# Kernel optimization log

Measured on AMD Instinct MI355X. Metric: run time of the kernel, lower is better.

Reference implementation:

```python
import jax, jax.numpy as jnp
import numpy as np

N_NODES = 100_000
N_FACES = 200_000
N_EDGES1 = 800_000
N_TRIP = 500_000
H = 64
GEO_IN = 10 + 2 * 23  # 56
N_INTER = 3
DEPTH = 3  # finaldepth; total SPNN layers = DEPTH + 1
PI = float(np.pi)
EPS = 1e-5


def setup_inputs() -> dict:
    key = jax.random.key(0)
    ks = jax.random.split(key, 12)
    s = 0.05
    input_feature = jax.random.normal(ks[0], (N_NODES, H), jnp.float32)
    coords = jax.random.normal(ks[1], (N_NODES, 3), jnp.float32)
    face_norm = jax.random.normal(ks[2], (N_FACES, 3), jnp.float32)
    face_x = jax.random.normal(ks[3], (N_FACES, 23), jnp.float32)
    edge_whichface = jax.random.randint(ks[4], (N_EDGES1,), 0, N_FACES)
    edge_index_2rd = jax.random.randint(ks[5], (3, N_TRIP), 0, N_NODES)
    edx_ij = jax.random.randint(ks[6], (N_TRIP,), 0, N_EDGES1)
    edx_rand = jax.random.randint(ks[7], (N_TRIP,), 0, N_EDGES1)
    edx_jk = jnp.where(jnp.arange(N_TRIP) % 2 == 0, edx_ij, edx_rand)
    att = jnp.ones((2,), jnp.float32)
    W_geo = jax.random.normal(ks[8], (H, GEO_IN), jnp.float32) * s
    b_geo = jnp.zeros((H,), jnp.float32)
    g_geo = jnp.ones((H,), jnp.float32)
    be_geo = jnp.zeros((H,), jnp.float32)
    spnn_W0 = jax.random.normal(ks[9], (N_INTER, 2, H, 4 * H), jnp.float32) * s
    spnn_b0 = jnp.zeros((N_INTER, 2, H), jnp.float32)
    spnn_Wr = jax.random.normal(ks[10], (N_INTER, 2, DEPTH, H, H), jnp.float32) * s
    spnn_br = jnp.zeros((N_INTER, 2, DEPTH, H), jnp.float32)
    bn_g = jnp.ones((N_INTER, 2, DEPTH + 1, H), jnp.float32)
    bn_b = jnp.zeros((N_INTER, 2, DEPTH + 1, H), jnp.float32)
    return dict(input_feature=input_feature, coords=coords, face_norm=face_norm,
                face_x=face_x, att=att, W_geo=W_geo, b_geo=b_geo, g_geo=g_geo,
                be_geo=be_geo, spnn_W0=spnn_W0, spnn_b0=spnn_b0, spnn_Wr=spnn_Wr,
                spnn_br=spnn_br, bn_g=bn_g, bn_b=bn_b,
                edge_whichface=edge_whichface, edge_index_2rd=edge_index_2rd,
                edx_jk=edx_jk, edx_ij=edx_ij)


def _bn(x, g, b):
    # BatchNorm1d, training mode (batch stats, biased variance)
    mean = x.mean(0)
    var = ((x - mean) ** 2).mean(0)
    return (x - mean) * jax.lax.rsqrt(var + EPS) * g + b


def _masked_bn(x, mf, g, b):
    # BatchNorm over only the masked rows (original code runs BN on x_i[mask]);
    # applied to all rows, masked rows selected afterward -> identical math.
    cnt = jnp.maximum(mf.sum(), 1.0)
    mean = (x * mf).sum(0) / cnt
    var = (((x - mean) ** 2) * mf).sum(0) / cnt
    return (x - mean) * jax.lax.rsqrt(var + EPS) * g + b


def _angle(v1, v2):
    c = jnp.cross(v1, v2)
    return jnp.arctan2(jnp.linalg.norm(c, axis=1), (v1 * v2).sum(1))


def reference(input_feature, coords, face_norm, face_x, att, W_geo, b_geo,
              g_geo, be_geo, spnn_W0, spnn_b0, spnn_Wr, spnn_br, bn_g, bn_b,
              edge_whichface, edge_index_2rd, edx_jk, edx_ij):
    i, j, k = edge_index_2rd
    f_ij = edge_whichface[edx_ij]
    f_jk = edge_whichface[edx_jk]
    # angle_face is computed then multiplied by 0 in the original
    angle_face = (PI - _angle(face_norm[f_ij], face_norm[f_jk])) * 0.0
    cj, ci, ck = coords[j], coords[i], coords[k]
    d_ij = jnp.linalg.norm(cj - ci, axis=1)
    d_jk = jnp.linalg.norm(cj - ck, axis=1)
    theta = _angle(cj - ci, ck - cj)
    same_face = f_ij == f_jk
    geo = jnp.concatenate([d_ij[:, None], d_jk[:, None], theta[:, None],
                           angle_face[:, None], cj, ci,
                           face_x[f_ij], face_x[f_jk]], axis=-1)  # [E, 56]
    geo = jax.nn.relu(_bn(geo @ W_geo.T + b_geo, g_geo, be_geo))  # [E, H]

    nf = input_feature
    masks = [same_face, ~same_face]
    outs = []
    for t in range(N_INTER):
        xcat = jnp.concatenate([nf[i], nf[j], nf[k], geo], axis=-1)  # [E, 4H]
        x_out = jnp.zeros((xcat.shape[0], H), xcat.dtype)
        for bi in range(2):
            mf = masks[bi].astype(xcat.dtype)[:, None]
            x = jax.nn.relu(_masked_bn(xcat @ spnn_W0[t, bi].T + spnn_b0[t, bi],
                                       mf, bn_g[t, bi, 0], bn_b[t, bi, 0]))
            for l in range(DEPTH):
                x = jax.nn.relu(_masked_bn(x @ spnn_Wr[t, bi, l].T + spnn_br[t, bi, l],
                                           mf, bn_g[t, bi, l + 1], bn_b[t, bi, l + 1]))
            x = jax.nn.leaky_relu(x) * att[bi]
            x_out = x_out + x * mf
        nf = jax.ops.segment_sum(x_out, i, num_segments=N_NODES)
        outs.append(nf)
    return jnp.stack(outs)  # [N_INTER, N, H] (list in original)
```

## Files before the change

kernel.cpp:

```cpp
#include <hip/hip_runtime.h>

#define E_TRIP 500000
#define EPAD   500224
#define NTILE64 (EPAD/64)
#define NBLK256 (EPAD/256)
#define NBLK    1954
#define NN 100000
#define EPSF 1e-5f
#define RSTAT 64

typedef _Float16 f16;
typedef _Float16 f16x8 __attribute__((ext_vector_type(8)));
typedef float f32x4 __attribute__((ext_vector_type(4)));

__global__ __launch_bounds__(256) void k_count(const int* __restrict__ ewf,
    const int* __restrict__ exij, const int* __restrict__ exjk,
    unsigned char* __restrict__ biedge, int* __restrict__ cb0)
{
  __shared__ int wcnt[4];
  int e = blockIdx.x*256 + threadIdx.x;
  bool active = e < E_TRIP;
  int b = 0;
  if (active) {
    int fij = ewf[exij[e]];
    int fjk = ewf[exjk[e]];
    b = (fij == fjk) ? 0 : 1;
    biedge[e] = (unsigned char)b;
  }
  unsigned long long m0 = __ballot(active && b==0);
  int lane = threadIdx.x & 63, wv = threadIdx.x >> 6;
  if (lane == 0) wcnt[wv] = (int)__popcll(m0);
  __syncthreads();
  if (threadIdx.x == 0) cb0[blockIdx.x] = wcnt[0] + wcnt[1] + wcnt[2] + wcnt[3];
}

__global__ __launch_bounds__(1024) void k_scanb(const int* __restrict__ cb0,
    int* __restrict__ base0, int* __restrict__ base1, int* __restrict__ sc)
{
  __shared__ int s[2048];
  int tid = threadIdx.x;
  int i0 = tid, i1 = tid + 1024;
  s[i0] = (i0 < NBLK) ? cb0[i0] : 0;
  s[i1] = (i1 < NBLK) ? cb0[i1] : 0;
  __syncthreads();
  for (int off = 1; off < 2048; off <<= 1) {
    int v0 = (i0 >= off) ? s[i0 - off] : 0;
    int v1 = (i1 >= off) ? s[i1 - off] : 0;
    __syncthreads();
    s[i0] += v0; s[i1] += v1;
    __syncthreads();
  }
  int c0 = s[NBLK-1];
  int c0p = (c0 + 63) & ~63;
  if (tid == 0) { sc[4] = c0; sc[5] = c0p; sc[6] = E_TRIP - c0; }
  for (int i = tid; i < NBLK; i += 1024) {
    int incl = s[i];
    int ex0 = incl - cb0[i];
    int active_before = i*256; if (active_before > E_TRIP) active_before = E_TRIP;
    base0[i] = ex0;
    base1[i] = c0p + (active_before - ex0);
  }
}

__global__ __launch_bounds__(256) void k_partition(const unsigned char* __restrict__ biedge,
    const int* __restrict__ eidx, const int* __restrict__ base0, const int* __restrict__ base1,
    int* __restrict__ epos, int* __restrict__ ip, int* __restrict__ jp, int* __restrict__ kp)
{
  __shared__ int w0[4], w1[4];
  int e = blockIdx.x*256 + threadIdx.x;
  bool active = e < E_TRIP;
  int b = active ? (int)biedge[e] : 0;
  unsigned long long m0 = __ballot(active && b==0);
  unsigned long long m1 = __ballot(active && b==1);
  int lane = threadIdx.x & 63, wv = threadIdx.x >> 6;
  if (lane == 0) { w0[wv] = (int)__popcll(m0); w1[wv] = (int)__popcll(m1); }
  __syncthreads();
  int off0 = 0, off1 = 0;
  #pragma unroll
  for (int w = 0; w < 4; w++) if (w < wv) { off0 += w0[w]; off1 += w1[w]; }
  if (active) {
    unsigned long long m = b ? m1 : m0;
    unsigned pre = __builtin_amdgcn_mbcnt_lo((unsigned)m, 0u);
    pre = __builtin_amdgcn_mbcnt_hi((unsigned)(m >> 32), pre);
    int base = b ? (base1[blockIdx.x] + off1) : (base0[blockIdx.x] + off0);
    int pos = base + (int)pre;
    epos[pos] = e;
    ip[pos] = eidx[e];
    jp[pos] = eidx[E_TRIP + e];
    kp[pos] = eidx[2*E_TRIP + e];
  }
}

__global__ __launch_bounds__(256) void k_cvt(const float* __restrict__ W0,
    const float* __restrict__ Wr, const float* __restrict__ nf,
    f16* __restrict__ W0h, f16* __restrict__ Wrh, f16* __restrict__ nfh)
{
  int i = blockIdx.x*256 + threadIdx.x;
  if (i < 98304) W0h[i] = (f16)W0[i];
  else if (i < 98304 + 73728) Wrh[i - 98304] = (f16)Wr[i - 98304];
  else { int j = i - 172032; if (j < NN*64) nfh[j] = (f16)nf[j]; }
}

__global__ __launch_bounds__(256) void k_hist(const int* __restrict__ ip,
    const int* __restrict__ sc, int* __restrict__ cnt)
{
  int p = blockIdx.x*256 + threadIdx.x;
  int c0 = sc[4], c0p = sc[5], c1 = sc[6];
  bool valid = (p < c0) || (p >= c0p && p < c0p + c1);
  if (valid) atomicAdd(&cnt[ip[p]], 1);
}

__global__ __launch_bounds__(512) void k_scan1(const int* __restrict__ cnt,
    int* __restrict__ start, int* __restrict__ btot)
{
  __shared__ int s[512];
  int tid = threadIdx.x;
  int g = blockIdx.x*512 + tid;
  int x = (g < NN) ? cnt[g] : 0;
  s[tid] = x; __syncthreads();
  #pragma unroll
  for (int off = 1; off < 512; off <<= 1) {
    int v = (tid >= off) ? s[tid-off] : 0;
    __syncthreads();
    s[tid] += v;
    __syncthreads();
  }
  if (g < NN) start[g] = s[tid] - x;
  if (tid == 511) btot[blockIdx.x] = s[511];
}

__global__ __launch_bounds__(256) void k_scan2(int* __restrict__ btot)
{
  __shared__ int s[256];
  int tid = threadIdx.x;
  int x = (tid < 196) ? btot[tid] : 0;
  s[tid] = x; __syncthreads();
  #pragma unroll
  for (int off = 1; off < 256; off <<= 1) {
    int v = (tid >= off) ? s[tid-off] : 0;
    __syncthreads();
    s[tid] += v;
    __syncthreads();
  }
  if (tid < 196) btot[tid] = s[tid] - x;
}

__global__ __launch_bounds__(512) void k_scan3(int* __restrict__ start,
    int* __restrict__ cur, const int* __restrict__ btot, const int* __restrict__ sc)
{
  int tid = threadIdx.x;
  int g = blockIdx.x*512 + tid;
  if (g < NN) {
    int v = start[g] + btot[blockIdx.x];
    start[g] = v;
    cur[g] = v;
  }
  if (g == 0) start[NN] = sc[4] + sc[6];
}

__global__ __launch_bounds__(256) void k_place(const int* __restrict__ ip,
    const int* __restrict__ sc, int* __restrict__ cur, int* __restrict__ dperm)
{
  int p = blockIdx.x*256 + threadIdx.x;
  int c0 = sc[4], c0p = sc[5], c1 = sc[6];
  bool valid = (p < c0) || (p >= c0p && p < c0p + c1);
  if (valid) {
    int pos = atomicAdd(&cur[ip[p]], 1);
    dperm[pos] = p;
  }
}

__global__ __launch_bounds__(256) void k_geo(
    const float* __restrict__ coords, const float* __restrict__ facex,
    const int* __restrict__ ewf, const int* __restrict__ exij, const int* __restrict__ exjk,
    const float* __restrict__ Wgeo, const float* __restrict__ bgeo,
    const int* __restrict__ sc, const int* __restrict__ epos,
    const int* __restrict__ ip, const int* __restrict__ jp, const int* __restrict__ kp,
    f16* __restrict__ zgeo, float* __restrict__ gstats)
{
  __shared__ f16 lds[256*72];
  __shared__ float sstat[64][2];
  int tid = threadIdx.x;
  int base = blockIdx.x*256;
  int c0 = sc[4], c0p = sc[5], c1 = sc[6];
  if (tid < 128) ((float*)sstat)[tid] = 0.f;
  {
    int p = base + tid;
    bool valid = (p < c0) || (p >= c0p && p < c0p + c1);
    f16* lrow = lds + tid*72;
    if (valid) {
      int e = epos[p];
      int ii = ip[p], jj = jp[p], kk = kp[p];
      float cix = coords[ii*3+0], ciy = coords[ii*3+1], ciz = coords[ii*3+2];
      float cjx = coords[jj*3+0], cjy = coords[jj*3+1], cjz = coords[jj*3+2];
      float ckx = coords[kk*3+0], cky = coords[kk*3+1], ckz = coords[kk*3+2];
      float v1x = cjx-cix, v1y = cjy-ciy, v1z = cjz-ciz;
      float v2x = ckx-cjx, v2y = cky-cjy, v2z = ckz-cjz;
      float dij = sqrtf(v1x*v1x + v1y*v1y + v1z*v1z);
      float djk = sqrtf(v2x*v2x + v2y*v2y + v2z*v2z);
      float cx = v1y*v2z - v1z*v2y;
      float cy = v1z*v2x - v1x*v2z;
      float cz = v1x*v2y - v1y*v2x;
      float theta = atan2f(sqrtf(cx*cx+cy*cy+cz*cz), v1x*v2x+v1y*v2y+v1z*v2z);
      lrow[0]=(f16)dij; lrow[1]=(f16)djk; lrow[2]=(f16)theta; lrow[3]=(f16)0.f;
      lrow[4]=(f16)cjx; lrow[5]=(f16)cjy; lrow[6]=(f16)cjz;
      lrow[7]=(f16)cix; lrow[8]=(f16)ciy; lrow[9]=(f16)ciz;
      int fij = ewf[exij[e]], fjk = ewf[exjk[e]];
      const float* fx1 = facex + (size_t)fij*23;
      const float* fx2 = facex + (size_t)fjk*23;
      for (int c = 0; c < 23; c++) lrow[10+c] = (f16)fx1[c];
      for (int c = 0; c < 23; c++) lrow[33+c] = (f16)fx2[c];
      for (int c = 56; c < 64; c++) lrow[c] = (f16)0.f;
    } else {
      for (int c = 0; c < 64; c++) lrow[c] = (f16)0.f;
    }
  }
  __syncthreads();
  int wv = tid>>6, lane = tid&63, lg = lane>>4, lr = lane&15;
  f16x8 Bf[4][2];
  #pragma unroll
  for (int nt = 0; nt < 4; nt++) {
    #pragma unroll
    for (int ks = 0; ks < 2; ks++) {
      int n = nt*16 + lr;
      int kb = ks*32 + lg*8;
      f16x8 w;
      if (kb < 56) {
        float4 w0 = *(const float4*)(Wgeo + n*56 + kb);
        float4 w1 = *(const float4*)(Wgeo + n*56 + kb + 4);
        w[0]=(f16)w0.x; w[1]=(f16)w0.y; w[2]=(f16)w0.z; w[3]=(f16)w0.w;
        w[4]=(f16)w1.x; w[5]=(f16)w1.y; w[6]=(f16)w1.z; w[7]=(f16)w1.w;
      } else {
        #pragma unroll
        for (int j2 = 0; j2 < 8; j2++) w[j2] = (f16)0.f;
      }
      Bf[nt][ks] = w;
    }
  }
  float ssum[4] = {0,0,0,0}, ssq[4] = {0,0,0,0};
  for (int mt = 0; mt < 4; mt++) {
    int rbase = wv*64 + mt*16;
    f16x8 A0 = *(const f16x8*)(lds + (rbase+lr)*72 + lg*8);
    f16x8 A1 = *(const f16x8*)(lds + (rbase+lr)*72 + 32 + lg*8);
    f32x4 acc[4];
    #pragma unroll
    for (int nt = 0; nt < 4; nt++) { acc[nt][0]=0.f; acc[nt][1]=0.f; acc[nt][2]=0.f; acc[nt][3]=0.f; }
    #pragma unroll
    for (int nt = 0; nt < 4; nt++) {
      acc[nt] = __builtin_amdgcn_mfma_f32_16x16x32_f16(A0, Bf[nt][0], acc[nt], 0, 0, 0);
      acc[nt] = __builtin_amdgcn_mfma_f32_16x16x32_f16(A1, Bf[nt][1], acc[nt], 0, 0, 0);
    }
    #pragma unroll
    for (int nt = 0; nt < 4; nt++) {
      int n = nt*16 + lr;
      float bg = bgeo[n];
      #pragma unroll
      for (int rg = 0; rg < 4; rg++) {
        int rloc = rbase + lg*4 + rg;
        int p = base + rloc;
        bool valid = (p < c0) || (p >= c0p && p < c0p + c1);
        float z = valid ? (acc[nt][rg] + bg) : 0.f;
        ssum[nt] += z; ssq[nt] += z*z;
        lds[rloc*72 + n] = (f16)z;
      }
    }
  }
  #pragma unroll
  for (int nt = 0; nt < 4; nt++) {
    float v = ssum[nt]; v += __shfl_xor(v, 16); v += __shfl_xor(v, 32);
    float w = ssq[nt];  w += __shfl_xor(w, 16); w += __shfl_xor(w, 32);
    if (lane < 16) { atomicAdd(&sstat[nt*16+lane][0], v); atomicAdd(&sstat[nt*16+lane][1], w); }
  }
  __syncthreads();
  {
    int p = base + tid;
    #pragma unroll
    for (int c = 0; c < 8; c++) {
      f16x8 v = *(const f16x8*)(lds + tid*72 + c*8);
      *(f16x8*)(zgeo + (size_t)p*64 + c*8) = v;
    }
  }
  if (tid < 128) {
    float v = ((float*)sstat)[tid];
    if (v != 0.f) atomicAdd(&gstats[(blockIdx.x & (RSTAT-1))*256 + tid], v);
  }
}

__global__ __launch_bounds__(256) void k_layer0(
    const f16* __restrict__ nfsrc, const f16* __restrict__ zgeo,
    const f16* __restrict__ W0p, const float* __restrict__ b0p,
    const float* __restrict__ g_geo, const float* __restrict__ be_geo,
    const float* __restrict__ geostats, float* __restrict__ outstats,
    const int* __restrict__ sc, const int* __restrict__ ip,
    const int* __restrict__ jp, const int* __restrict__ kp,
    f16* __restrict__ z0)
{
  __shared__ f16 lds[64*264];
  __shared__ float geoscale[64], geoshift[64];
  __shared__ float sstat[2][64][2];
  int tid = threadIdx.x;
  int c0 = sc[4], c0p = sc[5], c1 = sc[6];
  if (tid < 64) {
    float s = 0.f, sq = 0.f;
    #pragma unroll 8
    for (int r = 0; r < RSTAT; r++) {
      s  += geostats[r*256 + tid*2];
      sq += geostats[r*256 + tid*2 + 1];
    }
    float mean = s * (1.f/(float)E_TRIP);
    float var  = sq * (1.f/(float)E_TRIP) - mean*mean;
    float rstd = rsqrtf(var + EPSF);
    float scl = g_geo[tid]*rstd;
    geoscale[tid] = scl;
    geoshift[tid] = be_geo[tid] - mean*scl;
  }
  ((float*)sstat)[tid] = 0.f;
  __syncthreads();
  int wv = tid>>6, lane = tid&63, lg = lane>>4, lr = lane&15;
  float s0sum[4]={0,0,0,0}, s0sq[4]={0,0,0,0}, s1sum[4]={0,0,0,0}, s1sq[4]={0,0,0,0};
  for (int tile = blockIdx.x; tile < NTILE64; tile += gridDim.x) {
    int rowbase = tile*64;
    int branch = (rowbase >= c0p) ? 1 : 0;
    {
      int r = tid >> 2, q = tid & 3;
      int p = rowbase + r;
      bool valid = (p < c0) || (p >= c0p && p < c0p + c1);
      f16* rowp = lds + r*264 + q*64;
      if (q < 3) {
        if (valid) {
          int idx = (q==0 ? ip : (q==1 ? jp : kp))[p];
          const f16* src = nfsrc + (size_t)idx*64;
          #pragma unroll
          for (int c = 0; c < 8; c++) *(f16x8*)(rowp + c*8) = *(const f16x8*)(src + c*8);
        } else {
          f16x8 u;
          #pragma unroll
          for (int j2 = 0; j2 < 8; j2++) u[j2] = (f16)0.f;
          #pragma unroll
          for (int c = 0; c < 8; c++) *(f16x8*)(rowp + c*8) = u;
        }
      } else {
        if (valid) {
          const f16* zg = zgeo + (size_t)p*64;
          #pragma unroll
          for (int c = 0; c < 8; c++) {
            f16x8 raw = *(const f16x8*)(zg + c*8);
            f16x8 u;
            #pragma unroll
            for (int j2 = 0; j2 < 8; j2++) {
              int f = c*8 + j2;
              float x = fmaxf((float)raw[j2]*geoscale[f] + geoshift[f], 0.f);
              u[j2] = (f16)x;
            }
            *(f16x8*)(rowp + c*8) = u;
          }
        } else {
          f16x8 u;
          #pragma unroll
          for (int j2 = 0; j2 < 8; j2++) u[j2] = (f16)0.f;
          #pragma unroll
          for (int c = 0; c < 8; c++) *(f16x8*)(rowp + c*8) = u;
        }
      }
    }
    __syncthreads();
    {
      int r0 = wv*16;
      const f16* Wb = W0p + branch*16384;
      f32x4 acc[4];
      #pragma unroll
      for (int nt = 0; nt < 4; nt++) { acc[nt][0]=0.f; acc[nt][1]=0.f; acc[nt][2]=0.f; acc[nt][3]=0.f; }
      #pragma unroll
      for (int ks = 0; ks < 8; ks++) {
        f16x8 A = *(const f16x8*)(lds + (r0+lr)*264 + (ks*4+lg)*8);
        #pragma unroll
        for (int nt = 0; nt < 4; nt++) {
          f16x8 B = *(const f16x8*)(Wb + (nt*16+lr)*256 + ks*32 + lg*8);
          acc[nt] = __builtin_amdgcn_mfma_f32_16x16x32_f16(A, B, acc[nt], 0, 0, 0);
        }
      }
      #pragma unroll
      for (int nt = 0; nt < 4; nt++) {
        int n = nt*16 + lr;
        float bias = b0p[branch*64 + n];
        #pragma unroll
        for (int rg = 0; rg < 4; rg++) {
          int rloc = r0 + lg*4 + rg;
          int p = rowbase + rloc;
          bool valid = (p < c0) || (p >= c0p && p < c0p + c1);
          float z = valid ? (acc[nt][rg] + bias) : 0.f;
          if (branch == 0) { s0sum[nt] += z; s0sq[nt] += z*z; }
          else             { s1sum[nt] += z; s1sq[nt] += z*z; }
          lds[rloc*264 + n] = (f16)z;
        }
      }
    }
    __syncthreads();
    {
      int r = tid>>2, q = tid&3;
      int p = rowbase + r;
      f16x8 v0 = *(const f16x8*)(lds + r*264 + q*16);
      f16x8 v1 = *(const f16x8*)(lds + r*264 + q*16 + 8);
      *(f16x8*)(z0 + (size_t)p*64 + q*16) = v0;
      *(f16x8*)(z0 + (size_t)p*64 + q*16 + 8) = v1;
    }
    __syncthreads();
  }
  #pragma unroll
  for (int nt = 0; nt < 4; nt++) {
    float v, w;
    v = s0sum[nt]; v += __shfl_xor(v,16); v += __shfl_xor(v,32);
    w = s0sq[nt];  w += __shfl_xor(w,16); w += __shfl_xor(w,32);
    if (lane < 16) { atomicAdd(&sstat[0][nt*16+lane][0], v); atomicAdd(&sstat[0][nt*16+lane][1], w); }
    v = s1sum[nt]; v += __shfl_xor(v,16); v += __shfl_xor(v,32);
    w = s1sq[nt];  w += __shfl_xor(w,16); w += __shfl_xor(w,32);
    if (lane < 16) { atomicAdd(&sstat[1][nt*16+lane][0], v); atomicAdd(&sstat[1][nt*16+lane][1], w); }
  }
  __syncthreads();
  {
    float v = ((float*)sstat)[tid];
    if (v != 0.f) atomicAdd(&outstats[(blockIdx.x & (RSTAT-1))*256 + tid], v);
  }
}

__global__ __launch_bounds__(256) void k_hidden(
    const f16* __restrict__ zin, f16* __restrict__ zout,
    const f16* __restrict__ Wp, const float* __restrict__ biasp,
    const float* __restrict__ bngp, const float* __restrict__ bnbp,
    const float* __restrict__ instats, float* __restrict__ outstats,
    const int* __restrict__ sc)
{
  __shared__ float lscale[2][64], lshift[2][64];
  __shared__ float sstat[2][64][2];
  __shared__ f16 ldso[4][16*72];
  int tid = threadIdx.x;
  int c0 = sc[4], c0p = sc[5], c1 = sc[6];
  if (tid < 128) {
    int b = tid>>6, n = tid&63;
    int cb = b ? c1 : c0; if (cb < 1) cb = 1;
    float inv = 1.f/(float)cb;
    int idx = (b*64+n)*2;
    float s = 0.f, sq = 0.f;
    #pragma unroll 8
    for (int r = 0; r < RSTAT; r++) {
      s  += instats[r*256 + idx];
      sq += instats[r*256 + idx + 1];
    }
    float mean = s*inv, var = sq*inv - mean*mean;
    float rstd = rsqrtf(var + EPSF);
    float scl = bngp[b*256+n]*rstd;
    lscale[b][n] = scl;
    lshift[b][n] = bnbp[b*256+n] - mean*scl;
  }
  ((float*)sstat)[tid] = 0.f;
  __syncthreads();
  int wv = tid>>6, lane = tid&63, lg = lane>>4, lr = lane&15;
  f16* myldso = ldso[wv];
  float s0sum[4]={0,0,0,0}, s0sq[4]={0,0,0,0}, s1sum[4]={0,0,0,0}, s1sq[4]={0,0,0,0};
  for (int tile = blockIdx.x; tile < NTILE64; tile += gridDim.x) {
    int rowbase = tile*64;
    int branch = (rowbase >= c0p) ? 1 : 0;
    int rgl = rowbase + wv*16 + lr;
    f16x8 Af[2];
    #pragma unroll
    for (int ks = 0; ks < 2; ks++) {
      f16x8 raw = *(const f16x8*)(zin + (size_t)rgl*64 + ks*32 + lg*8);
      f16x8 A;
      #pragma unroll
      for (int j2 = 0; j2 < 8; j2++) {
        int f = ks*32 + lg*8 + j2;
        float x = fmaxf((float)raw[j2]*lscale[branch][f] + lshift[branch][f], 0.f);
        A[j2] = (f16)x;
      }
      Af[ks] = A;
    }
    f32x4 acc[4];
    #pragma unroll
    for (int nt = 0; nt < 4; nt++) { acc[nt][0]=0.f; acc[nt][1]=0.f; acc[nt][2]=0.f; acc[nt][3]=0.f; }
    #pragma unroll
    for (int ks = 0; ks < 2; ks++) {
      #pragma unroll
      for (int nt = 0; nt < 4; nt++) {
        f16x8 B = *(const f16x8*)(Wp + branch*12288 + (nt*16+lr)*64 + ks*32 + lg*8);
        acc[nt] = __builtin_amdgcn_mfma_f32_16x16x32_f16(Af[ks], B, acc[nt], 0, 0, 0);
      }
    }
    #pragma unroll
    for (int nt = 0; nt < 4; nt++) {
      int n = nt*16 + lr;
      float bias = biasp[branch*192 + n];
      #pragma unroll
      for (int rg = 0; rg < 4; rg++) {
        int rloc = lg*4 + rg;
        int p = rowbase + wv*16 + rloc;
        bool valid = (p < c0) || (p >= c0p && p < c0p + c1);
        float z = valid ? (acc[nt][rg] + bias) : 0.f;
        if (branch == 0) { s0sum[nt] += z; s0sq[nt] += z*z; }
        else             { s1sum[nt] += z; s1sq[nt] += z*z; }
        myldso[rloc*72 + n] = (f16)z;
      }
    }
    {
      int r2 = lane>>2, q = lane&3;
      int p2 = rowbase + wv*16 + r2;
      f16x8 v0 = *(const f16x8*)(myldso + r2*72 + q*8);
      f16x8 v1 = *(const f16x8*)(myldso + r2*72 + 32 + q*8);
      *(f16x8*)(zout + (size_t)p2*64 + q*8) = v0;
      *(f16x8*)(zout + (size_t)p2*64 + 32 + q*8) = v1;
    }
  }
  #pragma unroll
  for (int nt = 0; nt < 4; nt++) {
    float v, w;
    v = s0sum[nt]; v += __shfl_xor(v,16); v += __shfl_xor(v,32);
    w = s0sq[nt];  w += __shfl_xor(w,16); w += __shfl_xor(w,32);
    if (lane < 16) { atomicAdd(&sstat[0][nt*16+lane][0], v); atomicAdd(&sstat[0][nt*16+lane][1], w); }
    v = s1sum[nt]; v += __shfl_xor(v,16); v += __shfl_xor(v,32);
    w = s1sq[nt];  w += __shfl_xor(w,16); w += __shfl_xor(w,32);
    if (lane < 16) { atomicAdd(&sstat[1][nt*16+lane][0], v); atomicAdd(&sstat[1][nt*16+lane][1], w); }
  }
  __syncthreads();
  {
    float v = ((float*)sstat)[tid];
    if (v != 0.f) atomicAdd(&outstats[(blockIdx.x & (RSTAT-1))*256 + tid], v);
  }
}

__global__ __launch_bounds__(256) void k_scatter(
    const f16* __restrict__ z3, const float* __restrict__ att,
    const float* __restrict__ bngp, const float* __restrict__ bnbp,
    const float* __restrict__ instats, const int* __restrict__ sc,
    const int* __restrict__ start, const int* __restrict__ dperm,
    float* __restrict__ outt, f16* __restrict__ nfh)
{
  __shared__ float lscale[2][64], lshift[2][64];
  int tid = threadIdx.x;
  int c0p = sc[5];
  {
    int c0 = sc[4], c1 = sc[6];
    if (tid < 128) {
      int b = tid>>6, n = tid&63;
      int cb = b ? c1 : c0; if (cb < 1) cb = 1;
      float inv = 1.f/(float)cb;
      int idx = (b*64+n)*2;
      float s = 0.f, sq = 0.f;
      #pragma unroll 8
      for (int r = 0; r < RSTAT; r++) {
        s  += instats[r*256 + idx];
        sq += instats[r*256 + idx + 1];
      }
      float mean = s*inv, var = sq*inv - mean*mean;
      float rstd = rsqrtf(var + EPSF);
      float scl = bngp[b*256+n]*rstd;
      lscale[b][n] = scl;
      lshift[b][n] = bnbp[b*256+n] - mean*scl;
    }
  }
  __syncthreads();
  int gid = blockIdx.x*256 + tid;
  int n = gid >> 3, q = gid & 7;
  if (n >= NN) return;
  int s = start[n];
  int e = start[n+1];
  float a0 = att[0], a1 = att[1];
  float acc[8] = {0,0,0,0,0,0,0,0};
  float sc0[8], sh0[8], sc1[8], sh1[8];
  #pragma unroll
  for (int j2 = 0; j2 < 8; j2++) {
    int f = q*8 + j2;
    sc0[j2] = lscale[0][f]; sh0[j2] = lshift[0][f];
    sc1[j2] = lscale[1][f]; sh1[j2] = lshift[1][f];
  }
  for (int t = s; t < e; t++) {
    int p = dperm[t];
    int b = (p >= c0p) ? 1 : 0;
    float a = b ? a1 : a0;
    f16x8 raw = *(const f16x8*)(z3 + (size_t)p*64 + q*8);
    #pragma unroll
    for (int j2 = 0; j2 < 8; j2++) {
      float x = (float)raw[j2]*(b ? sc1[j2] : sc0[j2]) + (b ? sh1[j2] : sh0[j2]);
      acc[j2] += fmaxf(x, 0.f) * a;
    }
  }
  float4 lo, hi;
  lo.x=acc[0]; lo.y=acc[1]; lo.z=acc[2]; lo.w=acc[3];
  hi.x=acc[4]; hi.y=acc[5]; hi.z=acc[6]; hi.w=acc[7];
  *(float4*)(outt + (size_t)n*64 + q*8) = lo;
  *(float4*)(outt + (size_t)n*64 + q*8 + 4) = hi;
  f16x8 h;
  #pragma unroll
  for (int j2 = 0; j2 < 8; j2++) h[j2] = (f16)acc[j2];
  *(f16x8*)(nfh + (size_t)n*64 + q*8) = h;
}

extern "C" void kernel_launch(void* const* d_in, const int* in_sizes, int n_in,
                              void* d_out, int out_size, void* d_ws, size_t ws_size,
                              hipStream_t stream)
{
  const float* input_feature = (const float*)d_in[0];
  const float* coords   = (const float*)d_in[1];
  const float* face_x   = (const float*)d_in[3];
  const float* att      = (const float*)d_in[4];
  const float* W_geo    = (const float*)d_in[5];
  const float* b_geo    = (const float*)d_in[6];
  const float* g_geo    = (const float*)d_in[7];
  const float* be_geo   = (const float*)d_in[8];
  const float* spnn_W0  = (const float*)d_in[9];
  const float* spnn_b0  = (const float*)d_in[10];
  const float* spnn_Wr  = (const float*)d_in[11];
  const float* spnn_br  = (const float*)d_in[12];
  const float* bn_g     = (const float*)d_in[13];
  const float* bn_b     = (const float*)d_in[14];
  const int* ewf  = (const int*)d_in[15];
  const int* eidx = (const int*)d_in[16];
  const int* exjk = (const int*)d_in[17];
  const int* exij = (const int*)d_in[18];
  float* out = (float*)d_out;
  char* ws = (char*)d_ws;

  size_t off = 0;
  auto take = [&](size_t bytes) -> char* {
    size_t o = off; off = (off + bytes + 255) & ~(size_t)255; return ws + o;
  };
  const size_t STATBUF = (size_t)RSTAT*256;
  int*   sc     = (int*)take(256);
  float* stats  = (float*)take(13*STATBUF*sizeof(float));
  int*   cb0    = (int*)take(sizeof(int)*2048);
  int*   base0  = (int*)take(sizeof(int)*2048);
  int*   base1  = (int*)take(sizeof(int)*2048);
  int*   cnt    = (int*)take(sizeof(int)*NN);
  int*   startn = (int*)take(sizeof(int)*(NN+1));
  int*   curn   = (int*)take(sizeof(int)*NN);
  int*   btot   = (int*)take(sizeof(int)*256);
  int*   dperm  = (int*)take(sizeof(int)*EPAD);
  unsigned char* biedge = (unsigned char*)take(E_TRIP);
  int* epos = (int*)take(sizeof(int)*EPAD);
  int* ip   = (int*)take(sizeof(int)*EPAD);
  int* jp   = (int*)take(sizeof(int)*EPAD);
  int* kp   = (int*)take(sizeof(int)*EPAD);
  f16* W0h  = (f16*)take(sizeof(f16)*3*2*64*256);
  f16* Wrh  = (f16*)take(sizeof(f16)*3*2*3*64*64);
  f16* nf16 = (f16*)take(sizeof(f16)*(size_t)NN*64);
  f16* zgeo = (f16*)take(sizeof(f16)*(size_t)EPAD*64);
  f16* zA   = (f16*)take(sizeof(f16)*(size_t)EPAD*64);
  f16* zB   = (f16*)take(sizeof(f16)*(size_t)EPAD*64);
  if (off > ws_size) return;

  hipMemsetAsync(sc, 0, 256, stream);
  hipMemsetAsync(stats, 0, 13*STATBUF*sizeof(float), stream);
  hipMemsetAsync(cnt, 0, sizeof(int)*NN, stream);

  k_count    <<<NBLK, 256, 0, stream>>>(ewf, exij, exjk, biedge, cb0);
  k_scanb    <<<1, 1024, 0, stream>>>(cb0, base0, base1, sc);
  k_partition<<<NBLK, 256, 0, stream>>>(biedge, eidx, base0, base1, epos, ip, jp, kp);
  k_cvt      <<<25673, 256, 0, stream>>>(spnn_W0, spnn_Wr, input_feature, W0h, Wrh, nf16);
  k_hist <<<1954, 256, 0, stream>>>(ip, sc, cnt);
  k_scan1<<<196, 512, 0, stream>>>(cnt, startn, btot);
  k_scan2<<<1, 256, 0, stream>>>(btot);
  k_scan3<<<196, 512, 0, stream>>>(startn, curn, btot, sc);
  k_place<<<1954, 256, 0, stream>>>(ip, sc, curn, dperm);

  k_geo      <<<NBLK256, 256, 0, stream>>>(coords, face_x, ewf, exij, exjk, W_geo, b_geo,
                                           sc, epos, ip, jp, kp, zgeo, stats);
  for (int t = 0; t < 3; t++) {
    float* outt = out + (size_t)t*NN*64;
    k_layer0<<<1024, 256, 0, stream>>>(nf16, zgeo,
        W0h + (size_t)t*2*64*256, spnn_b0 + t*2*64,
        g_geo, be_geo, stats, stats + (size_t)(1 + t*4)*STATBUF,
        sc, ip, jp, kp, zA);
    f16* zi = zA; f16* zo = zB;
    for (int h = 0; h < 3; h++) {
      k_hidden<<<2048, 256, 0, stream>>>(zi, zo,
          Wrh + (size_t)t*2*3*64*64 + (size_t)h*64*64,
          spnn_br + t*2*3*64 + h*64,
          bn_g + t*2*4*64 + h*64,
          bn_b + t*2*4*64 + h*64,
          stats + (size_t)(1 + t*4 + h)*STATBUF,
          stats + (size_t)(1 + t*4 + h + 1)*STATBUF,
          sc);
      f16* tmp = zi; zi = zo; zo = tmp;
    }
    k_scatter<<<(NN*8 + 255)/256, 256, 0, stream>>>(zi, att,
        bn_g + t*2*4*64 + 3*64, bn_b + t*2*4*64 + 3*64,
        stats + (size_t)(1 + t*4 + 3)*STATBUF, sc, startn, dperm, outt, nf16);
  }
}
```

Measured before the change: 1.387 ms.

## Sort triplets by (branch, node) key so scatter reads contiguous rows

Replaces the two-stage branch partition followed by a node-sorted permutation with a single counting sort keyed on branch*NN + node. The edge arrays come out grouped by branch and then by destination node, so the scatter kernel walks contiguous rows with no dperm indirection or per-row branch select. This also drops the partition kernel and vectorises the fp16 conversion kernel. The cost is a histogram and scan twice as large, and atomic-order placement within a node, which makes row order nondeterministic.

```diff
diff --git a/kernel.cpp b/kernel.cpp
--- a/kernel.cpp
+++ b/kernel.cpp
@@ -6,6 +6,7 @@
 #define NBLK256 (EPAD/256)
 #define NBLK    1954
 #define NN 100000
+#define NBIN (2*NN)
 #define EPSF 1e-5f
 #define RSTAT 64
 
@@ -34,8 +35,7 @@
   if (threadIdx.x == 0) cb0[blockIdx.x] = wcnt[0] + wcnt[1] + wcnt[2] + wcnt[3];
 }
 
-__global__ __launch_bounds__(1024) void k_scanb(const int* __restrict__ cb0,
-    int* __restrict__ base0, int* __restrict__ base1, int* __restrict__ sc)
+__global__ __launch_bounds__(1024) void k_scanb(const int* __restrict__ cb0, int* __restrict__ sc)
 {
   __shared__ int s[2048];
   int tid = threadIdx.x;
@@ -50,44 +50,10 @@
     s[i0] += v0; s[i1] += v1;
     __syncthreads();
   }
-  int c0 = s[NBLK-1];
-  int c0p = (c0 + 63) & ~63;
-  if (tid == 0) { sc[4] = c0; sc[5] = c0p; sc[6] = E_TRIP - c0; }
-  for (int i = tid; i < NBLK; i += 1024) {
-    int incl = s[i];
-    int ex0 = incl - cb0[i];
-    int active_before = i*256; if (active_before > E_TRIP) active_before = E_TRIP;
-    base0[i] = ex0;
-    base1[i] = c0p + (active_before - ex0);
-  }
-}
-
-__global__ __launch_bounds__(256) void k_partition(const unsigned char* __restrict__ biedge,
-    const int* __restrict__ eidx, const int* __restrict__ base0, const int* __restrict__ base1,
-    int* __restrict__ epos, int* __restrict__ ip, int* __restrict__ jp, int* __restrict__ kp)
-{
-  __shared__ int w0[4], w1[4];
-  int e = blockIdx.x*256 + threadIdx.x;
-  bool active = e < E_TRIP;
-  int b = active ? (int)biedge[e] : 0;
-  unsigned long long m0 = __ballot(active && b==0);
-  unsigned long long m1 = __ballot(active && b==1);
-  int lane = threadIdx.x & 63, wv = threadIdx.x >> 6;
-  if (lane == 0) { w0[wv] = (int)__popcll(m0); w1[wv] = (int)__popcll(m1); }
-  __syncthreads();
-  int off0 = 0, off1 = 0;
-  #pragma unroll
-  for (int w = 0; w < 4; w++) if (w < wv) { off0 += w0[w]; off1 += w1[w]; }
-  if (active) {
-    unsigned long long m = b ? m1 : m0;
-    unsigned pre = __builtin_amdgcn_mbcnt_lo((unsigned)m, 0u);
-    pre = __builtin_amdgcn_mbcnt_hi((unsigned)(m >> 32), pre);
-    int base = b ? (base1[blockIdx.x] + off1) : (base0[blockIdx.x] + off0);
-    int pos = base + (int)pre;
-    epos[pos] = e;
-    ip[pos] = eidx[e];
-    jp[pos] = eidx[E_TRIP + e];
-    kp[pos] = eidx[2*E_TRIP + e];
+  if (tid == 0) {
+    int c0 = s[NBLK-1];
+    int c0p = (c0 + 63) & ~63;
+    sc[4] = c0; sc[5] = c0p; sc[6] = E_TRIP - c0;
   }
 }
 
@@ -95,19 +61,31 @@
     const float* __restrict__ Wr, const float* __restrict__ nf,
     f16* __restrict__ W0h, f16* __restrict__ Wrh, f16* __restrict__ nfh)
 {
-  int i = blockIdx.x*256 + threadIdx.x;
-  if (i < 98304) W0h[i] = (f16)W0[i];
-  else if (i < 98304 + 73728) Wrh[i - 98304] = (f16)Wr[i - 98304];
-  else { int j = i - 172032; if (j < NN*64) nfh[j] = (f16)nf[j]; }
-}
-
-__global__ __launch_bounds__(256) void k_hist(const int* __restrict__ ip,
-    const int* __restrict__ sc, int* __restrict__ cnt)
-{
-  int p = blockIdx.x*256 + threadIdx.x;
-  int c0 = sc[4], c0p = sc[5], c1 = sc[6];
-  bool valid = (p < c0) || (p >= c0p && p < c0p + c1);
-  if (valid) atomicAdd(&cnt[ip[p]], 1);
+  int i = (blockIdx.x*256 + threadIdx.x) * 4;
+  if (i < 98304) {
+    float4 v = *(const float4*)(W0 + i);
+    W0h[i]=(f16)v.x; W0h[i+1]=(f16)v.y; W0h[i+2]=(f16)v.z; W0h[i+3]=(f16)v.w;
+  } else if (i < 172032) {
+    int j = i - 98304;
+    float4 v = *(const float4*)(Wr + j);
+    Wrh[j]=(f16)v.x; Wrh[j+1]=(f16)v.y; Wrh[j+2]=(f16)v.z; Wrh[j+3]=(f16)v.w;
+  } else {
+    int j = i - 172032;
+    if (j < NN*64) {
+      float4 v = *(const float4*)(nf + j);
+      nfh[j]=(f16)v.x; nfh[j+1]=(f16)v.y; nfh[j+2]=(f16)v.z; nfh[j+3]=(f16)v.w;
+    }
+  }
+}
+
+__global__ __launch_bounds__(256) void k_hist(const unsigned char* __restrict__ biedge,
+    const int* __restrict__ eidx, int* __restrict__ cnt)
+{
+  int e = blockIdx.x*256 + threadIdx.x;
+  if (e < E_TRIP) {
+    int key = (int)biedge[e]*NN + eidx[e];
+    atomicAdd(&cnt[key], 1);
+  }
 }
 
 __global__ __launch_bounds__(512) void k_scan1(const int* __restrict__ cnt,
@@ -116,7 +94,7 @@
   __shared__ int s[512];
   int tid = threadIdx.x;
   int g = blockIdx.x*512 + tid;
-  int x = (g < NN) ? cnt[g] : 0;
+  int x = (g < NBIN) ? cnt[g] : 0;
   s[tid] = x; __syncthreads();
   #pragma unroll
   for (int off = 1; off < 512; off <<= 1) {
@@ -125,24 +103,24 @@
     s[tid] += v;
     __syncthreads();
   }
-  if (g < NN) start[g] = s[tid] - x;
+  if (g < NBIN) start[g] = s[tid] - x;
   if (tid == 511) btot[blockIdx.x] = s[511];
 }
 
-__global__ __launch_bounds__(256) void k_scan2(int* __restrict__ btot)
-{
-  __shared__ int s[256];
-  int tid = threadIdx.x;
-  int x = (tid < 196) ? btot[tid] : 0;
+__global__ __launch_bounds__(512) void k_scan2(int* __restrict__ btot)
+{
+  __shared__ int s[512];
+  int tid = threadIdx.x;
+  int x = (tid < 391) ? btot[tid] : 0;
   s[tid] = x; __syncthreads();
   #pragma unroll
-  for (int off = 1; off < 256; off <<= 1) {
+  for (int off = 1; off < 512; off <<= 1) {
     int v = (tid >= off) ? s[tid-off] : 0;
     __syncthreads();
     s[tid] += v;
     __syncthreads();
   }
-  if (tid < 196) btot[tid] = s[tid] - x;
+  if (tid < 391) btot[tid] = s[tid] - x;
 }
 
 __global__ __launch_bounds__(512) void k_scan3(int* __restrict__ start,
@@ -150,23 +128,28 @@
 {
   int tid = threadIdx.x;
   int g = blockIdx.x*512 + tid;
-  if (g < NN) {
+  if (g < NBIN) {
     int v = start[g] + btot[blockIdx.x];
+    if (g >= NN) v += sc[5] - sc[4];
     start[g] = v;
     cur[g] = v;
   }
-  if (g == 0) start[NN] = sc[4] + sc[6];
-}
-
-__global__ __launch_bounds__(256) void k_place(const int* __restrict__ ip,
-    const int* __restrict__ sc, int* __restrict__ cur, int* __restrict__ dperm)
-{
-  int p = blockIdx.x*256 + threadIdx.x;
-  int c0 = sc[4], c0p = sc[5], c1 = sc[6];
-  bool valid = (p < c0) || (p >= c0p && p < c0p + c1);
-  if (valid) {
-    int pos = atomicAdd(&cur[ip[p]], 1);
-    dperm[pos] = p;
+  if (g == 0) start[NBIN] = sc[5] + sc[6];
+}
+
+__global__ __launch_bounds__(256) void k_place(const unsigned char* __restrict__ biedge,
+    const int* __restrict__ eidx, int* __restrict__ cur,
+    int* __restrict__ epos, int* __restrict__ ip, int* __restrict__ jp, int* __restrict__ kp)
+{
+  int e = blockIdx.x*256 + threadIdx.x;
+  if (e < E_TRIP) {
+    int i = eidx[e];
+    int key = (int)biedge[e]*NN + i;
+    int pos = atomicAdd(&cur[key], 1);
+    epos[pos] = e;
+    ip[pos] = i;
+    jp[pos] = eidx[E_TRIP + e];
+    kp[pos] = eidx[2*E_TRIP + e];
   }
 }
 
@@ -530,17 +513,18 @@
     const f16* __restrict__ z3, const float* __restrict__ att,
     const float* __restrict__ bngp, const float* __restrict__ bnbp,
     const float* __restrict__ instats, const int* __restrict__ sc,
-    const int* __restrict__ start, const int* __restrict__ dperm,
+    const int* __restrict__ astart,
     float* __restrict__ outt, f16* __restrict__ nfh)
 {
   __shared__ float lscale[2][64], lshift[2][64];
   int tid = threadIdx.x;
-  int c0p = sc[5];
+  int c0 = sc[4];
   {
-    int c0 = sc[4], c1 = sc[6];
+    int c0p = sc[5], c1 = sc[6];
+    (void)c0p; (void)c1;
     if (tid < 128) {
       int b = tid>>6, n = tid&63;
-      int cb = b ? c1 : c0; if (cb < 1) cb = 1;
+      int cb = b ? sc[6] : sc[4]; if (cb < 1) cb = 1;
       float inv = 1.f/(float)cb;
       int idx = (b*64+n)*2;
       float s = 0.f, sq = 0.f;
@@ -560,26 +544,31 @@
   int gid = blockIdx.x*256 + tid;
   int n = gid >> 3, q = gid & 7;
   if (n >= NN) return;
-  int s = start[n];
-  int e = start[n+1];
+  int s0 = astart[n];
+  int e0 = astart[n+1]; if (e0 > c0) e0 = c0;
+  int s1 = astart[NN+n];
+  int e1 = astart[NN+n+1];
   float a0 = att[0], a1 = att[1];
   float acc[8] = {0,0,0,0,0,0,0,0};
-  float sc0[8], sh0[8], sc1[8], sh1[8];
-  #pragma unroll
-  for (int j2 = 0; j2 < 8; j2++) {
-    int f = q*8 + j2;
-    sc0[j2] = lscale[0][f]; sh0[j2] = lshift[0][f];
-    sc1[j2] = lscale[1][f]; sh1[j2] = lshift[1][f];
-  }
-  for (int t = s; t < e; t++) {
-    int p = dperm[t];
-    int b = (p >= c0p) ? 1 : 0;
-    float a = b ? a1 : a0;
-    f16x8 raw = *(const f16x8*)(z3 + (size_t)p*64 + q*8);
+  float scb[8], shb[8];
+  #pragma unroll
+  for (int j2 = 0; j2 < 8; j2++) { scb[j2] = lscale[0][q*8+j2]; shb[j2] = lshift[0][q*8+j2]; }
+  for (int t = s0; t < e0; t++) {
+    f16x8 raw = *(const f16x8*)(z3 + (size_t)t*64 + q*8);
     #pragma unroll
     for (int j2 = 0; j2 < 8; j2++) {
-      float x = (float)raw[j2]*(b ? sc1[j2] : sc0[j2]) + (b ? sh1[j2] : sh0[j2]);
-      acc[j2] += fmaxf(x, 0.f) * a;
+      float x = (float)raw[j2]*scb[j2] + shb[j2];
+      acc[j2] += fmaxf(x, 0.f) * a0;
+    }
+  }
+  #pragma unroll
+  for (int j2 = 0; j2 < 8; j2++) { scb[j2] = lscale[1][q*8+j2]; shb[j2] = lshift[1][q*8+j2]; }
+  for (int t = s1; t < e1; t++) {
+    f16x8 raw = *(const f16x8*)(z3 + (size_t)t*64 + q*8);
+    #pragma unroll
+    for (int j2 = 0; j2 < 8; j2++) {
+      float x = (float)raw[j2]*scb[j2] + shb[j2];
+      acc[j2] += fmaxf(x, 0.f) * a1;
     }
   }
   float4 lo, hi;
@@ -626,13 +615,10 @@
   int*   sc     = (int*)take(256);
   float* stats  = (float*)take(13*STATBUF*sizeof(float));
   int*   cb0    = (int*)take(sizeof(int)*2048);
-  int*   base0  = (int*)take(sizeof(int)*2048);
-  int*   base1  = (int*)take(sizeof(int)*2048);
-  int*   cnt    = (int*)take(sizeof(int)*NN);
-  int*   startn = (int*)take(sizeof(int)*(NN+1));
-  int*   curn   = (int*)take(sizeof(int)*NN);
-  int*   btot   = (int*)take(sizeof(int)*256);
-  int*   dperm  = (int*)take(sizeof(int)*EPAD);
+  int*   cnt    = (int*)take(sizeof(int)*NBIN);
+  int*   astart = (int*)take(sizeof(int)*(NBIN+1));
+  int*   curn   = (int*)take(sizeof(int)*NBIN);
+  int*   btot   = (int*)take(sizeof(int)*512);
   unsigned char* biedge = (unsigned char*)take(E_TRIP);
   int* epos = (int*)take(sizeof(int)*EPAD);
   int* ip   = (int*)take(sizeof(int)*EPAD);
@@ -648,20 +634,19 @@
 
   hipMemsetAsync(sc, 0, 256, stream);
   hipMemsetAsync(stats, 0, 13*STATBUF*sizeof(float), stream);
-  hipMemsetAsync(cnt, 0, sizeof(int)*NN, stream);
-
-  k_count    <<<NBLK, 256, 0, stream>>>(ewf, exij, exjk, biedge, cb0);
-  k_scanb    <<<1, 1024, 0, stream>>>(cb0, base0, base1, sc);
-  k_partition<<<NBLK, 256, 0, stream>>>(biedge, eidx, base0, base1, epos, ip, jp, kp);
-  k_cvt      <<<25673, 256, 0, stream>>>(spnn_W0, spnn_Wr, input_feature, W0h, Wrh, nf16);
-  k_hist <<<1954, 256, 0, stream>>>(ip, sc, cnt);
-  k_scan1<<<196, 512, 0, stream>>>(cnt, startn, btot);
-  k_scan2<<<1, 256, 0, stream>>>(btot);
-  k_scan3<<<196, 512, 0, stream>>>(startn, curn, btot, sc);
-  k_place<<<1954, 256, 0, stream>>>(ip, sc, curn, dperm);
-
-  k_geo      <<<NBLK256, 256, 0, stream>>>(coords, face_x, ewf, exij, exjk, W_geo, b_geo,
-                                           sc, epos, ip, jp, kp, zgeo, stats);
+  hipMemsetAsync(cnt, 0, sizeof(int)*NBIN, stream);
+
+  k_count <<<NBLK, 256, 0, stream>>>(ewf, exij, exjk, biedge, cb0);
+  k_scanb <<<1, 1024, 0, stream>>>(cb0, sc);
+  k_cvt   <<<6418, 256, 0, stream>>>(spnn_W0, spnn_Wr, input_feature, W0h, Wrh, nf16);
+  k_hist  <<<NBLK, 256, 0, stream>>>(biedge, eidx, cnt);
+  k_scan1 <<<391, 512, 0, stream>>>(cnt, astart, btot);
+  k_scan2 <<<1, 512, 0, stream>>>(btot);
+  k_scan3 <<<391, 512, 0, stream>>>(astart, curn, btot, sc);
+  k_place <<<NBLK, 256, 0, stream>>>(biedge, eidx, curn, epos, ip, jp, kp);
+
+  k_geo   <<<NBLK256, 256, 0, stream>>>(coords, face_x, ewf, exij, exjk, W_geo, b_geo,
+                                        sc, epos, ip, jp, kp, zgeo, stats);
   for (int t = 0; t < 3; t++) {
     float* outt = out + (size_t)t*NN*64;
     k_layer0<<<1024, 256, 0, stream>>>(nf16, zgeo,
@@ -682,6 +667,6 @@
     }
     k_scatter<<<(NN*8 + 255)/256, 256, 0, stream>>>(zi, att,
         bn_g + t*2*4*64 + 3*64, bn_b + t*2*4*64 + 3*64,
-        stats + (size_t)(1 + t*4 + 3)*STATBUF, sc, startn, dperm, outt, nf16);
-  }
-}
+        stats + (size_t)(1 + t*4 + 3)*STATBUF, sc, astart, outt, nf16);
+  }
+}
```

New measurement: 1.386 ms. About the same (-0.0%).
